# Kernel optimization log

Measured on AMD Instinct MI355X. Metric: run time of the kernel, lower is better.

Reference implementation:

```python
import jax, jax.numpy as jnp
import numpy as np

HIDDEN = 2048
N_HEADS = 8
N_KV_HEADS = 1
HEAD_DIM = 256
ROPE_THETA = 10000.0
B, S = 2, 2048


def setup_inputs() -> dict:
    key = jax.random.key(0)
    ks = jax.random.split(key, 6)
    sc = 0.02
    hidden_states = jax.random.normal(ks[0], (B, S, HIDDEN), dtype=jnp.float32)
    position_ids = jnp.broadcast_to(jnp.arange(S, dtype=jnp.int64 if jax.config.jax_enable_x64 else jnp.int32), (B, S))
    # additive causal mask: 0 on/below diagonal, large negative above
    causal = jnp.tril(jnp.ones((S, S), dtype=bool))
    attention_mask = jnp.where(causal, 0.0, -1e9).astype(jnp.float32)[None, None, :, :]
    attention_mask = jnp.broadcast_to(attention_mask, (B, 1, S, S))
    Wq = jax.random.normal(ks[1], (HIDDEN, N_HEADS * HEAD_DIM), dtype=jnp.float32) * sc
    Wk = jax.random.normal(ks[2], (HIDDEN, N_KV_HEADS * HEAD_DIM), dtype=jnp.float32) * sc
    Wv = jax.random.normal(ks[3], (HIDDEN, N_KV_HEADS * HEAD_DIM), dtype=jnp.float32) * sc
    Wo = jax.random.normal(ks[4], (N_HEADS * HEAD_DIM, HIDDEN), dtype=jnp.float32) * sc
    return {"hidden_states": hidden_states, "position_ids": position_ids,
            "attention_mask": attention_mask, "Wq": Wq, "Wk": Wk, "Wv": Wv, "Wo": Wo}


def _rotate_half(x):
    x1, x2 = jnp.split(x, 2, axis=-1)
    return jnp.concatenate([-x2, x1], axis=-1)


def _rope_cos_sin(position_ids, dtype):
    # inv_freq: [head_dim/2]
    inv_freq = 1.0 / (ROPE_THETA ** (jnp.arange(0, HEAD_DIM, 2, dtype=jnp.float32) / HEAD_DIM))
    # freqs: [B, S, head_dim/2]
    freqs = position_ids.astype(jnp.float32)[:, :, None] * inv_freq[None, None, :]
    emb = jnp.concatenate([freqs, freqs], axis=-1)  # [B, S, head_dim]
    return jnp.cos(emb).astype(dtype), jnp.sin(emb).astype(dtype)


def reference(hidden_states, position_ids, attention_mask, Wq, Wk, Wv, Wo):
    b, s, _ = hidden_states.shape
    # projections (bias=False)
    q = (hidden_states @ Wq).reshape(b, s, N_HEADS, HEAD_DIM).transpose(0, 2, 1, 3)      # [B,H,S,D]
    k = (hidden_states @ Wk).reshape(b, s, N_KV_HEADS, HEAD_DIM).transpose(0, 2, 1, 3)   # [B,Hk,S,D]
    v = (hidden_states @ Wv).reshape(b, s, N_KV_HEADS, HEAD_DIM).transpose(0, 2, 1, 3)
    cos, sin = _rope_cos_sin(position_ids, hidden_states.dtype)  # [B,S,D]
    cos, sin = cos[:, None], sin[:, None]  # [B,1,S,D]
    q = q * cos + _rotate_half(q) * sin
    k = k * cos + _rotate_half(k) * sin
    # repeat_kv for GQA
    n_rep = N_HEADS // N_KV_HEADS
    k = jnp.repeat(k, n_rep, axis=1)  # [B,H,S,D]
    v = jnp.repeat(v, n_rep, axis=1)
    scale = HEAD_DIM ** -0.5
    scores = jnp.einsum('bhqd,bhkd->bhqk', q, k) * scale + attention_mask
    attn_weights = jax.nn.softmax(scores.astype(jnp.float32), axis=-1).astype(q.dtype)
    attn_out = jnp.einsum('bhqk,bhkd->bhqd', attn_weights, v)
    attn_out = attn_out.transpose(0, 2, 1, 3).reshape(b, s, N_HEADS * HEAD_DIM)
    out = attn_out @ Wo
    return out, attn_weights
```

## Files before the change

### kernel.cpp

```cpp
#include <hip/hip_runtime.h>
#include <hip/hip_bf16.h>
#include <math.h>

typedef __attribute__((ext_vector_type(4))) float f32x4;
typedef __attribute__((ext_vector_type(8))) __bf16 bf16x8;
typedef __attribute__((ext_vector_type(8))) unsigned short u16x8;

#define HID    2048
#define NHEADS 8
#define HDIM   256
#define SEQ    2048
#define BATCH  2
#define ROWS   (BATCH*SEQ)
#define QKVN   (NHEADS*HDIM + 2*HDIM)
#define NBH    (BATCH*NHEADS)
#define NPTILE 32

#define GM_F32    0
#define GM_BF16   1
#define GM_SCORES 2

#define BIGNEG (-3.0e38f)

typedef __attribute__((address_space(1))) const void gvoid_t;
typedef __attribute__((address_space(3))) void lvoid_t;

__device__ __forceinline__ void gload16(const void* g, void* l){
  __builtin_amdgcn_global_load_lds((gvoid_t*)g, (lvoid_t*)l, 16, 0, 0);
}

__device__ __forceinline__ float bf2f(unsigned short u){
  union { unsigned int i; float f; } x; x.i = ((unsigned int)u) << 16; return x.f;
}
__device__ __forceinline__ unsigned short f2bf(float f){
  union { float f; unsigned int i; } x; x.f = f;
  unsigned int u = x.i;
  return (unsigned short)((u + 0x7FFFu + ((u >> 16) & 1u)) >> 16);
}

__global__ __launch_bounds__(256)
void k_f32_to_bf16(const float* __restrict__ src, unsigned short* __restrict__ dst){
  long i = ((long)blockIdx.x * 256 + threadIdx.x) * 16;
  f32x4 x0 = *(const f32x4*)(src + i);
  f32x4 x1 = *(const f32x4*)(src + i + 4);
  f32x4 x2 = *(const f32x4*)(src + i + 8);
  f32x4 x3 = *(const f32x4*)(src + i + 12);
  u16x8 w0, w1;
  #pragma unroll
  for (int j = 0; j < 4; ++j){
    w0[j]   = f2bf(x0[j]);
    w0[4+j] = f2bf(x1[j]);
    w1[j]   = f2bf(x2[j]);
    w1[4+j] = f2bf(x3[j]);
  }
  *(u16x8*)(dst + i)     = w0;
  *(u16x8*)(dst + i + 8) = w1;
}

__global__ __launch_bounds__(256)
void k_transpose(const float* __restrict__ src, unsigned short* __restrict__ dst,
                 int srcCols, int dstLd){
  __shared__ float t[32][33];
  int bx = blockIdx.x * 32;
  int by = blockIdx.y * 32;
  int tx = threadIdx.x & 31, ty = threadIdx.x >> 5;
  #pragma unroll
  for (int i = 0; i < 4; ++i){
    int rr = ty + i*8;
    t[rr][tx] = src[(long)(by + rr)*srcCols + bx + tx];
  }
  __syncthreads();
  #pragma unroll
  for (int i = 0; i < 4; ++i){
    int rr = ty + i*8;
    dst[(long)(bx + rr)*dstLd + by + tx] = f2bf(t[tx][rr]);
  }
}

__global__ __launch_bounds__(256)
void k_rope(const unsigned short* __restrict__ qkv, const int* __restrict__ pos_ids,
            unsigned short* __restrict__ Qb, unsigned short* __restrict__ Kb,
            unsigned short* __restrict__ VT){
  int row = blockIdx.x;
  int b = row >> 11, s = row & (SEQ - 1);
  float pos = (float)pos_ids[row];
  int tid = threadIdx.x;
  const unsigned short* r = qkv + (long)row * QKVN;

  #pragma unroll
  for (int it = 0; it < 4; ++it){
    int p = it*256 + tid;
    int d = p & 127, h = p >> 7;
    int col = h*HDIM + d;
    float inv = (float)exp((double)d * -0.07195578415606393);
    float ang = pos * inv;
    float sn, cs; sincosf(ang, &sn, &cs);
    float x0 = bf2f(r[col]), x1 = bf2f(r[col + 128]);
    Qb[(long)row*HID + col]       = f2bf(x0*cs - x1*sn);
    Qb[(long)row*HID + col + 128] = f2bf(x1*cs + x0*sn);
  }
  if (tid < 128){
    int d = tid;
    float inv = (float)exp((double)d * -0.07195578415606393);
    float ang = pos * inv;
    float sn, cs; sincosf(ang, &sn, &cs);
    float x0 = bf2f(r[HID + d]), x1 = bf2f(r[HID + d + 128]);
    Kb[(long)row*HDIM + d]       = f2bf(x0*cs - x1*sn);
    Kb[(long)row*HDIM + d + 128] = f2bf(x1*cs + x0*sn);
  }
  {
    int d = tid;
    VT[((long)b*HDIM + d)*SEQ + s] = r[HID + HDIM + d];
  }
}

__global__ __launch_bounds__(256)
void k_pvsm(float* __restrict__ S, const unsigned short* __restrict__ VT,
            unsigned short* __restrict__ AOb, const float* __restrict__ part){
  constexpr int QB = 32, BK = 64;
  int bh = blockIdx.x; int b = bh >> 3, h = bh & 7;
  int qtile = 63 - (int)blockIdx.z;
  int qbase = qtile * QB;
  int kceil = (qbase & ~63) + 64;
  int iters = kceil >> 6;

  float* Sh = S + (long)bh * SEQ * SEQ;
  const unsigned short* Vb = VT + (long)b * HDIM * SEQ;
  const float* pmb = part + (long)bh * NPTILE * SEQ;
  const float* plb = pmb + (long)NBH * NPTILE * SEQ;

  __shared__ unsigned short lA[QB*BK];
  __shared__ unsigned short lB[2*HDIM*BK];
  __shared__ float mlm[QB], mli[QB];

  int tid = threadIdx.x, lane = tid & 63, w = tid >> 6;
  int prow = tid >> 3, c8 = tid & 7;
  int vswz = ((lane & 7) ^ ((lane >> 3) & 7)) * 8;

  {
    int r = qbase + prow;
    float m = BIGNEG, l = 0.f;
    int nt = (r >> 6) + 1;
    for (int tc = c8; tc < nt; tc += 8){
      float mt = pmb[(long)tc*SEQ + r], lt = plb[(long)tc*SEQ + r];
      float nm = fmaxf(m, mt);
      l = l*__expf(m - nm) + lt*__expf(mt - nm);
      m = nm;
    }
    #pragma unroll
    for (int off = 1; off < 8; off <<= 1){
      float om = __shfl_xor(m, off), ol = __shfl_xor(l, off);
      float nm = fmaxf(m, om);
      l = l*__expf(m - nm) + ol*__expf(om - nm);
      m = nm;
    }
    if (c8 == 0){ mlm[prow] = m; mli[prow] = 1.0f / l; }
  }
  __syncthreads();

  float pm  = mlm[prow];
  float pil = mli[prow];
  int   rglob = qbase + prow;
  float* prowp = Sh + (long)rglob * SEQ;

  f32x4 acc[2][4];
  #pragma unroll
  for (int m = 0; m < 2; ++m)
    #pragma unroll
    for (int n = 0; n < 4; ++n)
      #pragma unroll
      for (int q = 0; q < 4; ++q) acc[m][n][q] = 0.f;

#define STAGE_V(k0_, buf_)                                                     \
  { _Pragma("unroll")                                                          \
    for (int t = 0; t < 8; ++t){                                               \
      int seg = w*8 + t;                                                       \
      const unsigned short* src = Vb + (long)(seg*8 + (lane >> 3))*SEQ + (k0_) + vswz; \
      gload16(src, (char*)lB + (buf_)*32768 + seg*1024);                       \
    } }

  f32x4 x0 = *(const f32x4*)(prowp + c8*8);
  f32x4 x1 = *(const f32x4*)(prowp + c8*8 + 4);
  STAGE_V(0, 0)
  int cur = 0;

  for (int it = 0; it < iters; ++it){
    int k0 = it * BK;
    asm volatile("s_waitcnt vmcnt(8)" ::: "memory");
    u16x8 u; f32x4 y0, y1;
    #pragma unroll
    for (int j = 0; j < 4; ++j){
      float p0 = (k0 + c8*8 + j     <= rglob) ? __expf(x0[j] - pm) * pil : 0.f;
      float p1 = (k0 + c8*8 + 4 + j <= rglob) ? __expf(x1[j] - pm) * pil : 0.f;
      y0[j] = p0; y1[j] = p1;
      u[j] = f2bf(p0); u[4+j] = f2bf(p1);
    }
    *(f32x4*)(prowp + k0 + c8*8)     = y0;
    *(f32x4*)(prowp + k0 + c8*8 + 4) = y1;
    { int kb = (c8*16) ^ ((prow & 7) << 4);
      *(u16x8*)((char*)lA + prow*128 + kb) = u; }
    if (it + 1 < iters){
      int k1 = k0 + BK;
      x0 = *(const f32x4*)(prowp + k1 + c8*8);
      x1 = *(const f32x4*)(prowp + k1 + c8*8 + 4);
      STAGE_V(k1, cur^1)
      asm volatile("s_waitcnt vmcnt(12)" ::: "memory");
    } else {
      asm volatile("s_waitcnt vmcnt(2)" ::: "memory");
    }
    asm volatile("s_waitcnt lgkmcnt(0)" ::: "memory");
    __builtin_amdgcn_s_barrier();

    const char* lBc = (const char*)lB + cur*32768;
    __builtin_amdgcn_s_setprio(1);
    #pragma unroll
    for (int kk = 0; kk < 2; ++kk){
      bf16x8 af[2];
      #pragma unroll
      for (int m = 0; m < 2; ++m){
        int row = m*16 + (lane & 15);
        int kb = (kk*64 + (lane >> 4)*16) ^ ((row & 7) << 4);
        af[m] = *(const bf16x8*)((const char*)lA + row*128 + kb);
      }
      #pragma unroll
      for (int n = 0; n < 4; ++n){
        int vr = w*64 + n*16 + (lane & 15);
        int kb = (kk*64 + (lane >> 4)*16) ^ ((vr & 7) << 4);
        bf16x8 bfr = *(const bf16x8*)(lBc + vr*128 + kb);
        acc[0][n] = __builtin_amdgcn_mfma_f32_16x16x32_bf16(af[0], bfr, acc[0][n], 0, 0, 0);
        acc[1][n] = __builtin_amdgcn_mfma_f32_16x16x32_bf16(af[1], bfr, acc[1][n], 0, 0, 0);
      }
    }
    __builtin_amdgcn_s_setprio(0);
    __builtin_amdgcn_s_barrier();
    cur ^= 1;
  }
#undef STAGE_V

  {
    f32x4 z4; z4[0]=0.f; z4[1]=0.f; z4[2]=0.f; z4[3]=0.f;
    for (int c0 = kceil; c0 < SEQ; c0 += BK){
      *(f32x4*)(prowp + c0 + c8*8)     = z4;
      *(f32x4*)(prowp + c0 + c8*8 + 4) = z4;
    }
  }

  #pragma unroll
  for (int m = 0; m < 2; ++m){
    #pragma unroll
    for (int ri = 0; ri < 4; ++ri){
      int row = qbase + m*16 + (lane >> 4)*4 + ri;
      long gr = (long)b*SEQ + row;
      #pragma unroll
      for (int n = 0; n < 4; ++n){
        int col = w*64 + n*16 + (lane & 15);
        AOb[gr*HID + h*HDIM + col] = f2bf(acc[m][n][ri]);
      }
    }
  }
}

template<int MODE>
__global__ __launch_bounds__(256)
void gemm_bt(const void* __restrict__ Av, const unsigned short* __restrict__ BT0,
             void* __restrict__ Cv,
             int M, int N, int K, int lda, int ldb, int ldc,
             long a_sb, long a_sh, long b_sb, long b_sh, long c_sb, long c_sh,
             int nH, float scale, float* __restrict__ part){
  constexpr int BM = 128, BN = 128, BK = 32;
  int m0 = blockIdx.x * BM, n0 = blockIdx.y * BN;
  if (MODE == GM_SCORES && n0 > m0 + BM - 1) return;

  int z = blockIdx.z;
  int zb = z / nH, zh = z % nH;

  const unsigned short* A16 = (const unsigned short*)Av + zb*a_sb + zh*a_sh;
  const unsigned short* BT = BT0 + zb*b_sb + zh*b_sh;

  __shared__ unsigned short lA[BM*BK];
  __shared__ unsigned short lB[BN*BK];

  int tid = threadIdx.x, lane = tid & 63, w = tid >> 6;
  int wr = w >> 1, wc = w & 1;
  int lrow = lane & 15, lk = (lane >> 4) * 8;

  f32x4 acc[4][4];
  #pragma unroll
  for (int m = 0; m < 4; ++m)
    #pragma unroll
    for (int n = 0; n < 4; ++n)
      #pragma unroll
      for (int q = 0; q < 4; ++q) acc[m][n][q] = 0.f;

  for (int k0 = 0; k0 < K; k0 += BK){
    #pragma unroll
    for (int t = 0; t < 2; ++t){
      int seg = w*2 + t;
      const unsigned short* src = A16 + (long)(m0 + seg*16 + (lane >> 2))*lda + k0 + (lane & 3)*8;
      gload16(src, &lA[seg*512]);
    }
    #pragma unroll
    for (int t = 0; t < 2; ++t){
      int seg = w*2 + t;
      const unsigned short* src = BT + (long)(n0 + seg*16 + (lane >> 2))*ldb + k0 + (lane & 3)*8;
      gload16(src, &lB[seg*512]);
    }
    __syncthreads();

    bf16x8 af[4], bfr[4];
    #pragma unroll
    for (int m = 0; m < 4; ++m)
      af[m] = *(const bf16x8*)&lA[(wr*64 + m*16 + lrow)*BK + lk];
    #pragma unroll
    for (int n = 0; n < 4; ++n)
      bfr[n] = *(const bf16x8*)&lB[(wc*64 + n*16 + lrow)*BK + lk];
    #pragma unroll
    for (int m = 0; m < 4; ++m)
      #pragma unroll
      for (int n = 0; n < 4; ++n)
        acc[m][n] = __builtin_amdgcn_mfma_f32_16x16x32_bf16(af[m], bfr[n], acc[m][n], 0, 0, 0);
    __syncthreads();
  }

  long cbase = zb*c_sb + zh*c_sh;
  if constexpr (MODE == GM_SCORES){
    int tc = (n0 + wc*64) >> 6;
    float* pm_out = part + ((long)z * NPTILE + tc) * SEQ;
    float* pl_out = pm_out + (long)NBH * NPTILE * SEQ;
    #pragma unroll
    for (int m = 0; m < 4; ++m){
      #pragma unroll
      for (int ri = 0; ri < 4; ++ri){
        int orow = m0 + wr*64 + m*16 + (lane >> 4)*4 + ri;
        float v[4]; bool ok[4];
        float mx = BIGNEG;
        #pragma unroll
        for (int n = 0; n < 4; ++n){
          int ocol = n0 + wc*64 + n*16 + (lane & 15);
          v[n] = acc[m][n][ri] * scale;
          ok[n] = (ocol <= orow);
          if (ok[n]){
            ((float*)Cv)[cbase + (long)orow*ldc + ocol] = v[n];
            mx = fmaxf(mx, v[n]);
          }
        }
        #pragma unroll
        for (int off = 8; off; off >>= 1) mx = fmaxf(mx, __shfl_xor(mx, off));
        float sm = 0.f;
        #pragma unroll
        for (int n = 0; n < 4; ++n) if (ok[n]) sm += __expf(v[n] - mx);
        #pragma unroll
        for (int off = 8; off; off >>= 1) sm += __shfl_xor(sm, off);
        if ((lane & 15) == 0){ pm_out[orow] = mx; pl_out[orow] = sm; }
      }
    }
  } else {
    #pragma unroll
    for (int m = 0; m < 4; ++m){
      #pragma unroll
      for (int ri = 0; ri < 4; ++ri){
        int orow = m0 + wr*64 + m*16 + (lane >> 4)*4 + ri;
        #pragma unroll
        for (int n = 0; n < 4; ++n){
          int ocol = n0 + wc*64 + n*16 + (lane & 15);
          float vv = acc[m][n][ri];
          if (MODE == GM_F32){
            ((float*)Cv)[cbase + (long)orow*ldc + ocol] = vv;
          } else {
            ((unsigned short*)Cv)[cbase + (long)orow*ldc + ocol] = f2bf(vv);
          }
        }
      }
    }
  }
}

extern "C" void kernel_launch(void* const* d_in, const int* in_sizes, int n_in,
                              void* d_out, int out_size, void* d_ws, size_t ws_size,
                              hipStream_t stream){
  const float* hs  = (const float*)d_in[0];
  const int*   pos = (const int*)  d_in[1];
  const float* Wq  = (const float*)d_in[3];
  const float* Wk  = (const float*)d_in[4];
  const float* Wv  = (const float*)d_in[5];
  const float* Wo  = (const float*)d_in[6];

  float* out  = (float*)d_out;
  float* Sbuf = out + (long)ROWS * HID;

  unsigned short* wsp   = (unsigned short*)d_ws;
  unsigned short* hsb   = wsp;
  unsigned short* wqkvT = hsb   + (long)ROWS*HID;
  unsigned short* woT   = wqkvT + (long)QKVN*HID;
  unsigned short* qkvb  = woT   + (long)HID*HID;
  unsigned short* Qb    = qkvb  + (long)ROWS*QKVN;
  unsigned short* Kb    = Qb    + (long)ROWS*HID;
  unsigned short* VT    = Kb    + (long)ROWS*HDIM;
  unsigned short* AOb   = VT    + (long)BATCH*HDIM*SEQ;

  float* part = (float*)hsb;

  k_f32_to_bf16<<<(ROWS*HID)/(256*16), 256, 0, stream>>>(hs, hsb);
  k_transpose<<<dim3(HID/32,  HID/32), 256, 0, stream>>>(Wq, wqkvT, HID, HID);
  k_transpose<<<dim3(HDIM/32, HID/32), 256, 0, stream>>>(Wk, wqkvT + (long)HID*HID, HDIM, HID);
  k_transpose<<<dim3(HDIM/32, HID/32), 256, 0, stream>>>(Wv, wqkvT + (long)(HID+HDIM)*HID, HDIM, HID);
  k_transpose<<<dim3(HID/32,  HID/32), 256, 0, stream>>>(Wo, woT, HID, HID);

  gemm_bt<GM_BF16><<<dim3(ROWS/128, QKVN/128, 1), 256, 0, stream>>>(
      hsb, wqkvT, qkvb, ROWS, QKVN, HID, HID, HID, QKVN,
      0, 0, 0, 0, 0, 0, 1, 1.f, nullptr);

  k_rope<<<ROWS, 256, 0, stream>>>(qkvb, pos, Qb, Kb, VT);

  gemm_bt<GM_SCORES><<<dim3(SEQ/128, SEQ/128, NBH), 256, 0, stream>>>(
      Qb, Kb, Sbuf, SEQ, SEQ, HDIM, HID, HDIM, SEQ,
      (long)SEQ*HID, (long)HDIM,
      (long)SEQ*HDIM, 0,
      (long)NHEADS*SEQ*SEQ, (long)SEQ*SEQ,
      NHEADS, 0.0625f, part);

  k_pvsm<<<dim3(NBH, 1, 64), 256, 0, stream>>>(Sbuf, VT, AOb, part);

  gemm_bt<GM_F32><<<dim3(ROWS/128, HID/128, 1), 256, 0, stream>>>(
      AOb, woT, out, ROWS, HID, HID, HID, HID, HID,
      0, 0, 0, 0, 0, 0, 1, 1.f, nullptr);
}
```

Measured before the change: 371.5 us.

## Add double-buffered 256x128 GEMM with swizzled LDS for projection GEMMs

Replaces the generic 128x128, BK=32 GEMM used for the QKV and output projections with a new 256x128 tile, BK=64 kernel using 512 threads. The new kernel double-buffers LDS with async global-to-LDS loads and partial vmcnt waits, so loads overlap MFMA work. It also XOR-swizzles the LDS layout to avoid bank conflicts. The scores GEMM is split into its own specialized kernel with constants folded in. Costs include higher LDS use, occupancy limited to one block per SM, and fewer blocks per grid.

```diff
diff --git a/kernel.cpp b/kernel.cpp
--- a/kernel.cpp
+++ b/kernel.cpp
@@ -15,10 +15,6 @@
 #define QKVN   (NHEADS*HDIM + 2*HDIM)
 #define NBH    (BATCH*NHEADS)
 #define NPTILE 32
-
-#define GM_F32    0
-#define GM_BF16   1
-#define GM_SCORES 2
 
 #define BIGNEG (-3.0e38f)
 
@@ -260,22 +256,114 @@
   }
 }
 
-template<int MODE>
+template<int OUTF32>
+__global__ __launch_bounds__(512, 1)
+void gemm256(const unsigned short* __restrict__ A16, const unsigned short* __restrict__ BT,
+             void* __restrict__ Cv, int lda, int ldb, int ldc, int K){
+  constexpr int BM = 256, BN = 128, BK = 64;
+  int m0 = blockIdx.x * BM, n0 = blockIdx.y * BN;
+
+  __shared__ unsigned short lA[2][BM*BK];
+  __shared__ unsigned short lB[2][BN*BK];
+
+  int tid = threadIdx.x, lane = tid & 63, w = tid >> 6;
+  int wr = w >> 1, wc = w & 1;
+  int srow = lane >> 3;
+  int vswz = ((lane & 7) ^ ((lane >> 3) & 7)) * 8;
+
+  f32x4 acc[4][4];
+  #pragma unroll
+  for (int m = 0; m < 4; ++m)
+    #pragma unroll
+    for (int n = 0; n < 4; ++n)
+      #pragma unroll
+      for (int q = 0; q < 4; ++q) acc[m][n][q] = 0.f;
+
+  int NT = K / BK;
+
+#define STAGE256(kt_, buf_)                                                    \
+  { int k0_ = (kt_) * BK;                                                      \
+    _Pragma("unroll")                                                          \
+    for (int t = 0; t < 4; ++t){                                               \
+      int seg = w*4 + t;                                                       \
+      const unsigned short* src = A16 + (long)(m0 + seg*8 + srow)*lda + k0_ + vswz; \
+      gload16(src, (char*)lA[buf_] + seg*1024);                                \
+    }                                                                          \
+    _Pragma("unroll")                                                          \
+    for (int t = 0; t < 2; ++t){                                               \
+      int seg = w*2 + t;                                                       \
+      const unsigned short* src = BT + (long)(n0 + seg*8 + srow)*ldb + k0_ + vswz; \
+      gload16(src, (char*)lB[buf_] + seg*1024);                                \
+    } }
+
+  STAGE256(0, 0)
+  STAGE256(1, 1)
+  int cur = 0;
+
+  for (int kt = 0; kt < NT; ++kt){
+    if (kt < NT - 1) asm volatile("s_waitcnt vmcnt(6)" ::: "memory");
+    else             asm volatile("s_waitcnt vmcnt(0)" ::: "memory");
+    __builtin_amdgcn_s_barrier();
+
+    const char* La = (const char*)lA[cur];
+    const char* Lb = (const char*)lB[cur];
+    __builtin_amdgcn_s_setprio(1);
+    #pragma unroll
+    for (int kk = 0; kk < 2; ++kk){
+      bf16x8 af[4], bfr[4];
+      #pragma unroll
+      for (int m = 0; m < 4; ++m){
+        int row = wr*64 + m*16 + (lane & 15);
+        int kb = (kk*64 + (lane >> 4)*16) ^ ((row & 7) << 4);
+        af[m] = *(const bf16x8*)(La + row*128 + kb);
+      }
+      #pragma unroll
+      for (int n = 0; n < 4; ++n){
+        int row = wc*64 + n*16 + (lane & 15);
+        int kb = (kk*64 + (lane >> 4)*16) ^ ((row & 7) << 4);
+        bfr[n] = *(const bf16x8*)(Lb + row*128 + kb);
+      }
+      #pragma unroll
+      for (int m = 0; m < 4; ++m)
+        #pragma unroll
+        for (int n = 0; n < 4; ++n)
+          acc[m][n] = __builtin_amdgcn_mfma_f32_16x16x32_bf16(af[m], bfr[n], acc[m][n], 0, 0, 0);
+    }
+    __builtin_amdgcn_s_setprio(0);
+    __builtin_amdgcn_s_barrier();
+    if (kt + 2 < NT) STAGE256(kt + 2, cur)
+    cur ^= 1;
+  }
+#undef STAGE256
+
+  #pragma unroll
+  for (int m = 0; m < 4; ++m){
+    #pragma unroll
+    for (int ri = 0; ri < 4; ++ri){
+      int orow = m0 + wr*64 + m*16 + (lane >> 4)*4 + ri;
+      #pragma unroll
+      for (int n = 0; n < 4; ++n){
+        int ocol = n0 + wc*64 + n*16 + (lane & 15);
+        float vv = acc[m][n][ri];
+        if (OUTF32) ((float*)Cv)[(long)orow*ldc + ocol] = vv;
+        else        ((unsigned short*)Cv)[(long)orow*ldc + ocol] = f2bf(vv);
+      }
+    }
+  }
+}
+
 __global__ __launch_bounds__(256)
-void gemm_bt(const void* __restrict__ Av, const unsigned short* __restrict__ BT0,
-             void* __restrict__ Cv,
-             int M, int N, int K, int lda, int ldb, int ldc,
-             long a_sb, long a_sh, long b_sb, long b_sh, long c_sb, long c_sh,
-             int nH, float scale, float* __restrict__ part){
+void gemm_scores(const unsigned short* __restrict__ Qb, const unsigned short* __restrict__ Kb,
+                 float* __restrict__ Cv, float* __restrict__ part, float scale){
   constexpr int BM = 128, BN = 128, BK = 32;
   int m0 = blockIdx.x * BM, n0 = blockIdx.y * BN;
-  if (MODE == GM_SCORES && n0 > m0 + BM - 1) return;
+  if (n0 > m0 + BM - 1) return;
 
   int z = blockIdx.z;
-  int zb = z / nH, zh = z % nH;
-
-  const unsigned short* A16 = (const unsigned short*)Av + zb*a_sb + zh*a_sh;
-  const unsigned short* BT = BT0 + zb*b_sb + zh*b_sh;
+  int zb = z >> 3;
+
+  const unsigned short* A16 = Qb + (long)zb*SEQ*HID + (long)(z & 7)*HDIM;
+  const unsigned short* BT  = Kb + (long)zb*SEQ*HDIM;
 
   __shared__ unsigned short lA[BM*BK];
   __shared__ unsigned short lB[BN*BK];
@@ -292,17 +380,17 @@
       #pragma unroll
       for (int q = 0; q < 4; ++q) acc[m][n][q] = 0.f;
 
-  for (int k0 = 0; k0 < K; k0 += BK){
+  for (int k0 = 0; k0 < HDIM; k0 += BK){
     #pragma unroll
     for (int t = 0; t < 2; ++t){
       int seg = w*2 + t;
-      const unsigned short* src = A16 + (long)(m0 + seg*16 + (lane >> 2))*lda + k0 + (lane & 3)*8;
+      const unsigned short* src = A16 + (long)(m0 + seg*16 + (lane >> 2))*HID + k0 + (lane & 3)*8;
       gload16(src, &lA[seg*512]);
     }
     #pragma unroll
     for (int t = 0; t < 2; ++t){
       int seg = w*2 + t;
-      const unsigned short* src = BT + (long)(n0 + seg*16 + (lane >> 2))*ldb + k0 + (lane & 3)*8;
+      const unsigned short* src = BT + (long)(n0 + seg*16 + (lane >> 2))*HDIM + k0 + (lane & 3)*8;
       gload16(src, &lB[seg*512]);
     }
     __syncthreads();
@@ -322,55 +410,35 @@
     __syncthreads();
   }
 
-  long cbase = zb*c_sb + zh*c_sh;
-  if constexpr (MODE == GM_SCORES){
-    int tc = (n0 + wc*64) >> 6;
-    float* pm_out = part + ((long)z * NPTILE + tc) * SEQ;
-    float* pl_out = pm_out + (long)NBH * NPTILE * SEQ;
-    #pragma unroll
-    for (int m = 0; m < 4; ++m){
-      #pragma unroll
-      for (int ri = 0; ri < 4; ++ri){
-        int orow = m0 + wr*64 + m*16 + (lane >> 4)*4 + ri;
-        float v[4]; bool ok[4];
-        float mx = BIGNEG;
-        #pragma unroll
-        for (int n = 0; n < 4; ++n){
-          int ocol = n0 + wc*64 + n*16 + (lane & 15);
-          v[n] = acc[m][n][ri] * scale;
-          ok[n] = (ocol <= orow);
-          if (ok[n]){
-            ((float*)Cv)[cbase + (long)orow*ldc + ocol] = v[n];
-            mx = fmaxf(mx, v[n]);
-          }
+  long cbase = (long)z * SEQ * SEQ;
+  int tc = (n0 + wc*64) >> 6;
+  float* pm_out = part + ((long)z * NPTILE + tc) * SEQ;
+  float* pl_out = pm_out + (long)NBH * NPTILE * SEQ;
+  #pragma unroll
+  for (int m = 0; m < 4; ++m){
+    #pragma unroll
+    for (int ri = 0; ri < 4; ++ri){
+      int orow = m0 + wr*64 + m*16 + (lane >> 4)*4 + ri;
+      float v[4]; bool ok[4];
+      float mx = BIGNEG;
+      #pragma unroll
+      for (int n = 0; n < 4; ++n){
+        int ocol = n0 + wc*64 + n*16 + (lane & 15);
+        v[n] = acc[m][n][ri] * scale;
+        ok[n] = (ocol <= orow);
+        if (ok[n]){
+          Cv[cbase + (long)orow*SEQ + ocol] = v[n];
+          mx = fmaxf(mx, v[n]);
         }
-        #pragma unroll
-        for (int off = 8; off; off >>= 1) mx = fmaxf(mx, __shfl_xor(mx, off));
-        float sm = 0.f;
-        #pragma unroll
-        for (int n = 0; n < 4; ++n) if (ok[n]) sm += __expf(v[n] - mx);
-        #pragma unroll
-        for (int off = 8; off; off >>= 1) sm += __shfl_xor(sm, off);
-        if ((lane & 15) == 0){ pm_out[orow] = mx; pl_out[orow] = sm; }
-      }
-    }
-  } else {
-    #pragma unroll
-    for (int m = 0; m < 4; ++m){
-      #pragma unroll
-      for (int ri = 0; ri < 4; ++ri){
-        int orow = m0 + wr*64 + m*16 + (lane >> 4)*4 + ri;
-        #pragma unroll
-        for (int n = 0; n < 4; ++n){
-          int ocol = n0 + wc*64 + n*16 + (lane & 15);
-          float vv = acc[m][n][ri];
-          if (MODE == GM_F32){
-            ((float*)Cv)[cbase + (long)orow*ldc + ocol] = vv;
-          } else {
-            ((unsigned short*)Cv)[cbase + (long)orow*ldc + ocol] = f2bf(vv);
-          }
-        }
-      }
+      }
+      #pragma unroll
+      for (int off = 8; off; off >>= 1) mx = fmaxf(mx, __shfl_xor(mx, off));
+      float sm = 0.f;
+      #pragma unroll
+      for (int n = 0; n < 4; ++n) if (ok[n]) sm += __expf(v[n] - mx);
+      #pragma unroll
+      for (int off = 8; off; off >>= 1) sm += __shfl_xor(sm, off);
+      if ((lane & 15) == 0){ pm_out[orow] = mx; pl_out[orow] = sm; }
     }
   }
 }
@@ -406,22 +474,16 @@
   k_transpose<<<dim3(HDIM/32, HID/32), 256, 0, stream>>>(Wv, wqkvT + (long)(HID+HDIM)*HID, HDIM, HID);
   k_transpose<<<dim3(HID/32,  HID/32), 256, 0, stream>>>(Wo, woT, HID, HID);
 
-  gemm_bt<GM_BF16><<<dim3(ROWS/128, QKVN/128, 1), 256, 0, stream>>>(
-      hsb, wqkvT, qkvb, ROWS, QKVN, HID, HID, HID, QKVN,
-      0, 0, 0, 0, 0, 0, 1, 1.f, nullptr);
+  gemm256<0><<<dim3(ROWS/256, QKVN/128), 512, 0, stream>>>(
+      hsb, wqkvT, qkvb, HID, HID, QKVN, HID);
 
   k_rope<<<ROWS, 256, 0, stream>>>(qkvb, pos, Qb, Kb, VT);
 
-  gemm_bt<GM_SCORES><<<dim3(SEQ/128, SEQ/128, NBH), 256, 0, stream>>>(
-      Qb, Kb, Sbuf, SEQ, SEQ, HDIM, HID, HDIM, SEQ,
-      (long)SEQ*HID, (long)HDIM,
-      (long)SEQ*HDIM, 0,
-      (long)NHEADS*SEQ*SEQ, (long)SEQ*SEQ,
-      NHEADS, 0.0625f, part);
+  gemm_scores<<<dim3(SEQ/128, SEQ/128, NBH), 256, 0, stream>>>(
+      Qb, Kb, Sbuf, part, 0.0625f);
 
   k_pvsm<<<dim3(NBH, 1, 64), 256, 0, stream>>>(Sbuf, VT, AOb, part);
 
-  gemm_bt<GM_F32><<<dim3(ROWS/128, HID/128, 1), 256, 0, stream>>>(
-      AOb, woT, out, ROWS, HID, HID, HID, HID, HID,
-      0, 0, 0, 0, 0, 0, 1, 1.f, nullptr);
-}
+  gemm256<1><<<dim3(ROWS/256, HID/128), 512, 0, stream>>>(
+      AOb, woT, out, HID, HID, HID, HID);
+}
```

Measured after the change: 376.1 us. No clear change (+1.2%).
